# Kernel tuning notes

Measured on AMD Instinct MI355X. Metric: run time of the kernel, lower is better.

Reference implementation:

```python
import jax, jax.numpy as jnp
import numpy as np

H, DH = 16, 64            # num heads, head dim
D = H * DH                # hidden size 1024
ALPHA, BW, A, R = 1.0, 1.0, 0.5, 1.0
D_INT = DH                # num_heads > 1 -> d_intrinsic = head_dim
EPS = 1e-12
CLIP = 1.0 - 1e-6         # keep acos (and its grad) finite


def setup_inputs() -> dict:
    key = jax.random.key(0)
    ks = jax.random.split(key, 5)
    w = lambda k: jax.random.normal(k, (D, D), jnp.float32) * 0.02
    return {
        "x": jax.random.normal(ks[0], (4, 1024, D), jnp.float32),
        "wq": w(ks[1]), "bq": jnp.zeros((D,), jnp.float32),
        "wk": w(ks[2]), "bk": jnp.zeros((D,), jnp.float32),
        "wv": w(ks[3]), "bv": jnp.zeros((D,), jnp.float32),
        "wo": w(ks[4]), "bo": jnp.zeros((D,), jnp.float32),
    }


def reference(x, wq, bq, wk, bk, wv, bv, wo, bo):
    B, S, _ = x.shape

    def heads(t):  # [B,S,D] -> [B,H,S,DH]
        return t.reshape(B, S, H, DH).transpose(0, 2, 1, 3)

    def l2norm(t):
        return t / jnp.maximum(jnp.linalg.norm(t, axis=-1, keepdims=True), EPS)

    q = l2norm(heads(x @ wq + bq))
    k = l2norm(heads(x @ wk + bk))
    v = heads(x @ wv + bv)

    # spherical geodesic distance
    dot = jnp.clip(jnp.einsum('bhqd,bhkd->bhqk', q, k), -CLIP, CLIP)
    g_dist = jnp.arccos(dot) * R

    # power-law kernel (alpha < 2 branch)
    attn_score = (1.0 + g_dist / jnp.sqrt(BW)) ** (-(D_INT + ALPHA))

    # bistochastic (Sinkhorn-like) normalization, a > 0 branch
    n_r = attn_score.sum(-1)   # [B,H,S] row sums
    n_c = attn_score.sum(-2)   # [B,H,S] col sums
    k_tilde = (n_r ** (-A))[..., :, None] * attn_score * (n_c ** (-A))[..., None, :]
    probs = k_tilde / jnp.maximum(k_tilde.sum(-1, keepdims=True), EPS)  # L1 row normalize

    out = jnp.einsum('bhqk,bhkd->bhqd', probs, v)
    out = out.transpose(0, 2, 1, 3).reshape(B, S, D)
    return out @ wo + bo
```

## Files before the change

kernel.cpp:

```cpp
#include <hip/hip_runtime.h>
#include <hip/hip_bf16.h>
#include <cstdint>
#include <cstddef>

#define BATCH  4
#define SEQ    1024
#define NHEAD  16
#define DHEAD  64
#define DMODEL 1024
#define NROWS  4096
#define BH     64
#define CLIPV  0.999999f
#define PEXP   65.0f

#define QOFF   133.5f
#define QK_    490.8988764f
#define QINV   0.0020370716f
#define QC     65535.5f

typedef _Float16 h16;
typedef _Float16 half8 __attribute__((ext_vector_type(8)));
typedef _Float16 half4 __attribute__((ext_vector_type(4)));
typedef __fp16   fp16x2 __attribute__((ext_vector_type(2)));
typedef float    f32x4 __attribute__((ext_vector_type(4)));

typedef const __attribute__((address_space(1))) void gas_void;
typedef __attribute__((address_space(3))) void las_void;
#define GLOAD_LDS16(g, l) \
    __builtin_amdgcn_global_load_lds((gas_void*)(g), (las_void*)(l), 16, 0, 0)

__device__ __forceinline__ float spfns_lg(float d) {
    d = __builtin_amdgcn_fmed3f(d, -CLIPV, CLIPV);
    float a = fabsf(d);
    float s = __builtin_amdgcn_sqrtf(1.0f - a);
    float p = -0.0012624911f;
    p = fmaf(p, a,  0.0066700901f);
    p = fmaf(p, a, -0.0170881256f);
    p = fmaf(p, a,  0.0308918810f);
    p = fmaf(p, a, -0.0501743046f);
    p = fmaf(p, a,  0.0889789874f);
    p = fmaf(p, a, -0.2145988016f);
    p = fmaf(p, a,  1.5707963050f);
    float r = s * p;
    float g = (d >= 0.0f) ? r : (3.14159265358979f - r);
    return __builtin_amdgcn_logf(1.0f + g);
}

__device__ __forceinline__ unsigned pk_h2(float lo, float hi) {
    fp16x2 v = __builtin_amdgcn_cvt_pkrtz(lo, hi);
    return __builtin_bit_cast(unsigned, v);
}

__global__ __launch_bounds__(256) void cvt_x(const float* __restrict__ x,
                                             h16* __restrict__ xh)
{
    size_t i = ((size_t)blockIdx.x * 256 + threadIdx.x) * 8;
    float4 a = *reinterpret_cast<const float4*>(&x[i]);
    float4 b = *reinterpret_cast<const float4*>(&x[i + 4]);
    half8 o;
    o[0]=(h16)a.x; o[1]=(h16)a.y; o[2]=(h16)a.z; o[3]=(h16)a.w;
    o[4]=(h16)b.x; o[5]=(h16)b.y; o[6]=(h16)b.z; o[7]=(h16)b.w;
    *reinterpret_cast<half8*>(&xh[i]) = o;
}

__global__ __launch_bounds__(256) void wtrans(const float* __restrict__ wq,
                                              const float* __restrict__ wk,
                                              const float* __restrict__ wv,
                                              const float* __restrict__ wo,
                                              h16* __restrict__ wt3,
                                              h16* __restrict__ wot)
{
    __shared__ float T[64][65];
    const int k0 = blockIdx.x * 64, d0 = blockIdx.y * 64, z = blockIdx.z;
    const float* src = (z==0)?wq:(z==1)?wk:(z==2)?wv:wo;
    h16* dst = (z==3) ? wot : (wt3 + (size_t)z * 1024 * 1024);
    const int t = threadIdx.x;

    #pragma unroll
    for (int p = 0; p < 4; ++p) {
        int k = (t >> 4) + p * 16;
        int c = (t & 15) * 4;
        float4 v = *reinterpret_cast<const float4*>(&src[(size_t)(k0 + k) * 1024 + d0 + c]);
        T[c + 0][k] = v.x; T[c + 1][k] = v.y; T[c + 2][k] = v.z; T[c + 3][k] = v.w;
    }
    __syncthreads();
    #pragma unroll
    for (int p = 0; p < 2; ++p) {
        int dl = (t >> 3) + p * 32;
        int c  = (t & 7) * 8;
        half8 o;
        #pragma unroll
        for (int e = 0; e < 8; ++e) o[e] = (h16)T[dl][c + e];
        *reinterpret_cast<half8*>(&dst[(size_t)(d0 + dl) * 1024 + k0 + c]) = o;
    }
}

__global__ __launch_bounds__(256) void gemm_f16(const h16* __restrict__ A,
                                                const h16* __restrict__ Bt,
                                                const float* __restrict__ b0,
                                                const float* __restrict__ b1,
                                                const float* __restrict__ b2,
                                                h16* __restrict__ oq,
                                                h16* __restrict__ ok,
                                                h16* __restrict__ ovt,
                                                float* __restrict__ of32,
                                                int mode)
{
    __shared__ __align__(16) h16 As[128][64];
    __shared__ __align__(16) h16 Bs[128][64];
    const int n0 = blockIdx.x * 128, d0 = blockIdx.y * 128;
    const int t = threadIdx.x, l = t & 63, w = t >> 6;
    const int wr = (w >> 1) * 64, wc = (w & 1) * 64;
    const int lr = l >> 3, lc8 = (l & 7) * 8;

    f32x4 acc[4][4];
    #pragma unroll
    for (int i = 0; i < 4; ++i)
        #pragma unroll
        for (int j = 0; j < 4; ++j) acc[i][j] = (f32x4){0.f,0.f,0.f,0.f};

    for (int k0 = 0; k0 < 1024; k0 += 64) {
        __syncthreads();
        #pragma unroll
        for (int q = 0; q < 4; ++q) {
            int r = w * 32 + q * 8;
            GLOAD_LDS16(&A[(size_t)(n0 + r + lr) * 1024 + k0 + lc8], &As[r][0]);
            GLOAD_LDS16(&Bt[(size_t)(d0 + r + lr) * 1024 + k0 + lc8], &Bs[r][0]);
        }
        __syncthreads();
        #pragma unroll
        for (int kk = 0; kk < 2; ++kk) {
            half8 a[4], b[4];
            #pragma unroll
            for (int fi = 0; fi < 4; ++fi)
                a[fi] = *reinterpret_cast<const half8*>(&As[wr + fi*16 + (l & 15)][((l >> 4) * 8) + kk * 32]);
            #pragma unroll
            for (int fj = 0; fj < 4; ++fj)
                b[fj] = *reinterpret_cast<const half8*>(&Bs[wc + fj*16 + (l & 15)][((l >> 4) * 8) + kk * 32]);
            #pragma unroll
            for (int fi = 0; fi < 4; ++fi)
                #pragma unroll
                for (int fj = 0; fj < 4; ++fj)
                    acc[fi][fj] = __builtin_amdgcn_mfma_f32_16x16x32_f16(a[fi], b[fj], acc[fi][fj], 0, 0, 0);
        }
    }

    #pragma unroll
    for (int fi = 0; fi < 4; ++fi) {
        #pragma unroll
        for (int fj = 0; fj < 4; ++fj) {
            int d = d0 + wc + fj * 16 + (l & 15);
            int s0n = n0 + wr + fi * 16 + ((l >> 4) << 2);
            if (mode == 0) {
                int mat = d >> 10, d1 = d & 1023, h = d1 >> 6, dh = d1 & 63;
                const float* bp = (mat == 0) ? b0 : (mat == 1) ? b1 : b2;
                float bias = bp[d1];
                if (mat == 2) {
                    int b = s0n >> 10, s0 = s0n & 1023;
                    half4 o;
                    #pragma unroll
                    for (int rr = 0; rr < 4; ++rr) o[rr] = (h16)(acc[fi][fj][rr] + bias);
                    *reinterpret_cast<half4*>(&ovt[(((size_t)(b * NHEAD + h)) * DHEAD + dh) * SEQ + s0]) = o;
                } else {
                    h16* dst = (mat == 0) ? oq : ok;
                    #pragma unroll
                    for (int rr = 0; rr < 4; ++rr) {
                        int n = s0n + rr, b = n >> 10, s = n & 1023;
                        dst[(((size_t)(b * NHEAD + h)) * SEQ + s) * DHEAD + dh] = (h16)(acc[fi][fj][rr] + bias);
                    }
                }
            } else {
                float bias = b0[d];
                #pragma unroll
                for (int rr = 0; rr < 4; ++rr) {
                    int n = s0n + rr;
                    of32[(size_t)n * DMODEL + d] = acc[fi][fj][rr] + bias;
                }
            }
        }
    }
}

__global__ __launch_bounds__(256) void l2norm_f16(h16* __restrict__ buf)
{
    const int t = threadIdx.x;
    size_t row = (size_t)blockIdx.x * 16 + (t >> 4);
    int c = (t & 15) * 4;
    half4 v = *reinterpret_cast<const half4*>(&buf[row * 64 + c]);
    float f0 = (float)v[0], f1 = (float)v[1], f2 = (float)v[2], f3 = (float)v[3];
    float s = f0*f0 + f1*f1 + f2*f2 + f3*f3;
    #pragma unroll
    for (int off = 1; off < 16; off <<= 1) s += __shfl_xor(s, off);
    float sc = __builtin_amdgcn_rcpf(fmaxf(__builtin_amdgcn_sqrtf(s), 1e-12f));
    half4 o;
    o[0] = (h16)(f0 * sc); o[1] = (h16)(f1 * sc); o[2] = (h16)(f2 * sc); o[3] = (h16)(f3 * sc);
    *reinterpret_cast<half4*>(&buf[row * 64 + c]) = o;
}

template<int CACHED>
__global__ __launch_bounds__(256) void passA(const h16* __restrict__ qh,
                                             const h16* __restrict__ kh,
                                             float* __restrict__ nc,
                                             unsigned* __restrict__ rm_u,
                                             int* __restrict__ gacc,
                                             unsigned short* __restrict__ Sw)
{
    __shared__ __align__(16) h16 Ks[32][72];
    __shared__ float red[4][32];
    const int t = threadIdx.x, l = t & 63, w = t >> 6;
    const int id  = blockIdx.y * 32 + blockIdx.x;
    const int nid = (id & 7) * 256 + (id >> 3);
    const int jt = nid & 31, bh = nid >> 5;
    const int j0 = jt * 32;

    {
        int r = t >> 3, c = (t & 7) * 8;
        *reinterpret_cast<half8*>(&Ks[r][c]) =
            *reinterpret_cast<const half8*>(&kh[(((size_t)bh * SEQ) + j0 + r) * DHEAD + c]);
    }
    __syncthreads();

    half8 kfr[2][2];
    #pragma unroll
    for (int f = 0; f < 2; ++f)
        #pragma unroll
        for (int kk = 0; kk < 2; ++kk)
            kfr[f][kk] = *reinterpret_cast<const half8*>(&Ks[f*16 + (l & 15)][((l >> 4) * 8) + kk * 32]);

    float ncacc[8];
    #pragma unroll
    for (int x = 0; x < 8; ++x) ncacc[x] = 0.f;

    const h16* qb = qh + ((size_t)bh * SEQ + w*16 + (l & 15)) * DHEAD + ((l >> 4) * 8);
    half8 nq0 = *reinterpret_cast<const half8*>(qb);
    half8 nq1 = *reinterpret_cast<const half8*>(qb + 32);

    for (int it = 0; it < 16; ++it) {
        half8 aq0 = nq0, aq1 = nq1;
        if (it < 15) {
            const h16* qn = qb + (size_t)(it + 1) * 64 * DHEAD;
            nq0 = *reinterpret_cast<const half8*>(qn);
            nq1 = *reinterpret_cast<const half8*>(qn + 32);
        }

        float mloc = 1e30f;
        #pragma unroll
        for (int f = 0; f < 2; ++f) {
            f32x4 cfr = (f32x4){0.f,0.f,0.f,0.f};
            cfr = __builtin_amdgcn_mfma_f32_16x16x32_f16(kfr[f][0], aq0, cfr, 0, 0, 0);
            cfr = __builtin_amdgcn_mfma_f32_16x16x32_f16(kfr[f][1], aq1, cfr, 0, 0, 0);
            unsigned uq[4];
            #pragma unroll
            for (int rr = 0; rr < 4; ++rr) {
                float lg = spfns_lg(cfr[rr]);
                float tt = lg * (-PEXP);
                ncacc[f*4 + rr] += __builtin_amdgcn_exp2f(tt);
                mloc = fminf(mloc, lg);
                if (CACHED) uq[rr] = (unsigned)fmaf(tt, QK_, QC);
            }
            if (CACHED) {
                uint2 pkw;
                pkw.x = uq[0] | (uq[1] << 16);
                pkw.y = uq[2] | (uq[3] << 16);
                size_t sidx = (((((size_t)(bh*16 + (jt >> 1))*16 + it)*4 + w)*4
                               + ((jt & 1)*2 + f)) << 8) + (size_t)l*4;
                *reinterpret_cast<uint2*>(&Sw[sidx]) = pkw;
            }
        }
        mloc = fminf(mloc, __shfl_xor(mloc, 16));
        mloc = fminf(mloc, __shfl_xor(mloc, 32));
        if (l < 16)
            atomicMin(&rm_u[(size_t)bh * SEQ + it*64 + w*16 + l], __float_as_uint(mloc));
    }

    #pragma unroll
    for (int x = 0; x < 8; ++x) {
        #pragma unroll
        for (int off = 1; off < 16; off <<= 1)
            ncacc[x] += __shfl_xor(ncacc[x], off);
    }
    if ((l & 15) == 0) {
        #pragma unroll
        for (int x = 0; x < 8; ++x)
            red[w][(x >> 2) * 16 + (l >> 4) * 4 + (x & 3)] = ncacc[x];
    }
    __syncthreads();
    if (t < 32) {
        float v = red[0][t] + red[1][t] + red[2][t] + red[3][t];
        nc[(size_t)bh * SEQ + j0 + t] = v;
        atomicAdd(gacc, (int)rintf(__builtin_amdgcn_logf(v) * 64.0f));
    }
}

__global__ __launch_bounds__(256) void ncprep(const float* __restrict__ nc,
                                              const unsigned* __restrict__ rm_u,
                                              const int* __restrict__ gacc,
                                              float* __restrict__ lcr,
                                              float* __restrict__ lrm)
{
    int i = blockIdx.x * 256 + threadIdx.x;
    float Lm = (float)(*gacc) / (65536.0f * 64.0f);
    lcr[i] = -0.5f * (__builtin_amdgcn_logf(nc[i]) - Lm);
    lrm[i] = -PEXP * __uint_as_float(rm_u[i]);
}

__global__ __launch_bounds__(256) void passB_c(const h16* __restrict__ vt,
                                               const float* __restrict__ lcr,
                                               const float* __restrict__ lrm,
                                               const unsigned short* __restrict__ Sw,
                                               h16* __restrict__ aoh)
{
    __shared__ __align__(16) h16 Vs[64][72];
    __shared__ __align__(16) h16 Ps[4][16][72];
    const int t = threadIdx.x, l = t & 63, w = t >> 6;
    const int id  = blockIdx.y * 16 + blockIdx.x;
    const int nid = (id & 7) * 128 + (id >> 3);
    const int it = nid & 15, bh = nid >> 4;
    const int i0 = it * 64;

    const float nlr = -lrm[(size_t)bh * SEQ + i0 + w*16 + (l & 15)] - QOFF;

    half8 ones8;
    {
        h16 ov = (h16)(((l & 15) == 0) ? 1.0f : 0.0f);
        #pragma unroll
        for (int e = 0; e < 8; ++e) ones8[e] = ov;
    }

    f32x4 pv[4];
    #pragma unroll
    for (int fd = 0; fd < 4; ++fd) pv[fd] = (f32x4){0.f,0.f,0.f,0.f};
    f32x4 pvden = (f32x4){0.f,0.f,0.f,0.f};

    const int sr = t >> 3, sc = (t & 7) * 8;
    const h16* vsrc = vt + ((size_t)bh * DHEAD + sr) * SEQ + sc;
    const float* lc_base = lcr + (size_t)bh * SEQ + (l >> 4) * 4;

    auto s_ptr = [&](int jc2, int fj) -> const uint2* {
        size_t sidx = (((((size_t)(bh*16 + jc2)*16 + it)*4 + w)*4 + fj) << 8) + (size_t)l*4;
        return reinterpret_cast<const uint2*>(&Sw[sidx]);
    };

    half8 vr0 = *reinterpret_cast<const half8*>(vsrc);
    half8 vr1 = *reinterpret_cast<const half8*>(vsrc + (size_t)32 * SEQ);
    uint2 sv[4];
    float4 lc[4];
    #pragma unroll
    for (int fj = 0; fj < 4; ++fj) {
        sv[fj] = *s_ptr(0, fj);
        lc[fj] = *reinterpret_cast<const float4*>(&lc_base[fj*16]);
    }

    for (int jc = 0; jc < 16; ++jc) {
        __syncthreads();
        *reinterpret_cast<half8*>(&Vs[sr][sc])      = vr0;
        *reinterpret_cast<half8*>(&Vs[sr + 32][sc]) = vr1;
        __syncthreads();

        if (jc < 15) {
            const h16* vn = vsrc + (jc + 1) * 64;
            vr0 = *reinterpret_cast<const half8*>(vn);
            vr1 = *reinterpret_cast<const half8*>(vn + (size_t)32 * SEQ);
        }

        #pragma unroll
        for (int fj = 0; fj < 4; ++fj) {
            float u0 = (float)(sv[fj].x & 0xffffu), u1 = (float)(sv[fj].x >> 16);
            float u2 = (float)(sv[fj].y & 0xffffu), u3 = (float)(sv[fj].y >> 16);
            float pp0 = __builtin_amdgcn_exp2f(fmaf(u0, QINV, lc[fj].x + nlr));
            float pp1 = __builtin_amdgcn_exp2f(fmaf(u1, QINV, lc[fj].y + nlr));
            float pp2 = __builtin_amdgcn_exp2f(fmaf(u2, QINV, lc[fj].z + nlr));
            float pp3 = __builtin_amdgcn_exp2f(fmaf(u3, QINV, lc[fj].w + nlr));
            uint2 pk;
            pk.x = pk_h2(pp0, pp1);
            pk.y = pk_h2(pp2, pp3);
            *reinterpret_cast<uint2*>(&Ps[w][l & 15][fj*16 + (l >> 4) * 4]) = pk;
        }
        if (jc < 15) {
            #pragma unroll
            for (int fj = 0; fj < 4; ++fj) {
                sv[fj] = *s_ptr(jc + 1, fj);
                lc[fj] = *reinterpret_cast<const float4*>(&lc_base[(jc + 1)*64 + fj*16]);
            }
        }

        half8 pa0 = *reinterpret_cast<const half8*>(&Ps[w][l & 15][((l >> 4) * 8)]);
        half8 pa1 = *reinterpret_cast<const half8*>(&Ps[w][l & 15][((l >> 4) * 8) + 32]);
        #pragma unroll
        for (int fd = 0; fd < 4; ++fd) {
            half8 vb0 = *reinterpret_cast<const half8*>(&Vs[fd*16 + (l & 15)][((l >> 4) * 8)]);
            half8 vb1 = *reinterpret_cast<const half8*>(&Vs[fd*16 + (l & 15)][((l >> 4) * 8) + 32]);
            pv[fd] = __builtin_amdgcn_mfma_f32_16x16x32_f16(pa0, vb0, pv[fd], 0, 0, 0);
            pv[fd] = __builtin_amdgcn_mfma_f32_16x16x32_f16(pa1, vb1, pv[fd], 0, 0, 0);
        }
        pvden = __builtin_amdgcn_mfma_f32_16x16x32_f16(pa0, ones8, pvden, 0, 0, 0);
        pvden = __builtin_amdgcn_mfma_f32_16x16x32_f16(pa1, ones8, pvden, 0, 0, 0);
    }

    const int b = bh >> 4, h = bh & 15;
    #pragma unroll
    for (int rr = 0; rr < 4; ++rr) {
        float ds = __shfl(pvden[rr], l & 48);
        float inv = __builtin_amdgcn_rcpf(ds);
        int s = i0 + w * 16 + ((l >> 4) << 2) + rr;
        #pragma unroll
        for (int fd = 0; fd < 4; ++fd) {
            aoh[((size_t)(b * SEQ + s)) * DMODEL + h * DHEAD + fd * 16 + (l & 15)] =
                (h16)(pv[fd][rr] * inv);
        }
    }
}

__global__ __launch_bounds__(256) void passB_r(const h16* __restrict__ qh,
                                               const h16* __restrict__ kh,
                                               const h16* __restrict__ vt,
                                               const float* __restrict__ lcr,
                                               const float* __restrict__ lrm,
                                               h16* __restrict__ aoh)
{
    __shared__ __align__(16) h16 Ks[64][72];
    __shared__ __align__(16) h16 Vs[64][72];
    __shared__ __align__(16) h16 Ps[4][16][72];
    __shared__ float lcr_s[64];
    __shared__ float lrm_s[64];

    const int it = blockIdx.x, bh = blockIdx.y;
    const int i0 = it * 64;
    const int t = threadIdx.x, l = t & 63, w = t >> 6;
    h16* Pflat = &Ps[0][0][0];

    #pragma unroll
    for (int p = 0; p < 2; ++p) {
        int r = (t >> 3) + p * 32, c = (t & 7) * 8;
        *reinterpret_cast<half8*>(&Pflat[r * 72 + c]) =
            *reinterpret_cast<const half8*>(&qh[(((size_t)bh * SEQ) + i0 + r) * DHEAD + c]);
    }
    if (t < 64) lrm_s[t] = lrm[(size_t)bh * SEQ + i0 + t];
    __syncthreads();

    half8 aq0 = *reinterpret_cast<const half8*>(&Pflat[(w*16 + (l & 15)) * 72 + ((l >> 4) * 8)]);
    half8 aq1 = *reinterpret_cast<const half8*>(&Pflat[(w*16 + (l & 15)) * 72 + ((l >> 4) * 8) + 32]);
    const float nlr = -lrm_s[w*16 + (l & 15)];

    half8 ones8;
    {
        h16 ov = (h16)(((l & 15) == 0) ? 1.0f : 0.0f);
        #pragma unroll
        for (int e = 0; e < 8; ++e) ones8[e] = ov;
    }

    f32x4 pv[4];
    #pragma unroll
    for (int fd = 0; fd < 4; ++fd) pv[fd] = (f32x4){0.f,0.f,0.f,0.f};
    f32x4 pvden = (f32x4){0.f,0.f,0.f,0.f};

    for (int jc = 0; jc < 16; ++jc) {
        const int j0 = jc * 64;
        __syncthreads();
        #pragma unroll
        for (int p = 0; p < 2; ++p) {
            int r = (t >> 3) + p * 32, c = (t & 7) * 8;
            *reinterpret_cast<half8*>(&Ks[r][c]) =
                *reinterpret_cast<const half8*>(&kh[(((size_t)bh * SEQ) + j0 + r) * DHEAD + c]);
            *reinterpret_cast<half8*>(&Vs[r][c]) =
                *reinterpret_cast<const half8*>(&vt[(((size_t)bh * DHEAD) + r) * SEQ + j0 + c]);
        }
        if (t < 64) lcr_s[t] = lcr[(size_t)bh * SEQ + j0 + t];
        __syncthreads();

        #pragma unroll
        for (int fj = 0; fj < 4; ++fj) {
            half8 kb0 = *reinterpret_cast<const half8*>(&Ks[fj*16 + (l & 15)][((l >> 4) * 8)]);
            half8 kb1 = *reinterpret_cast<const half8*>(&Ks[fj*16 + (l & 15)][((l >> 4) * 8) + 32]);
            f32x4 cfr = (f32x4){0.f,0.f,0.f,0.f};
            cfr = __builtin_amdgcn_mfma_f32_16x16x32_f16(kb0, aq0, cfr, 0, 0, 0);
            cfr = __builtin_amdgcn_mfma_f32_16x16x32_f16(kb1, aq1, cfr, 0, 0, 0);
            float4 lc4 = *reinterpret_cast<const float4*>(&lcr_s[fj*16 + (l >> 4) * 4]);
            float pp0 = __builtin_amdgcn_exp2f(fmaf(spfns_lg(cfr[0]), -PEXP, lc4.x + nlr));
            float pp1 = __builtin_amdgcn_exp2f(fmaf(spfns_lg(cfr[1]), -PEXP, lc4.y + nlr));
            float pp2 = __builtin_amdgcn_exp2f(fmaf(spfns_lg(cfr[2]), -PEXP, lc4.z + nlr));
            float pp3 = __builtin_amdgcn_exp2f(fmaf(spfns_lg(cfr[3]), -PEXP, lc4.w + nlr));
            uint2 pk;
            pk.x = pk_h2(pp0, pp1);
            pk.y = pk_h2(pp2, pp3);
            *reinterpret_cast<uint2*>(&Ps[w][l & 15][fj*16 + (l >> 4) * 4]) = pk;
        }

        half8 pa0 = *reinterpret_cast<const half8*>(&Ps[w][l & 15][((l >> 4) * 8)]);
        half8 pa1 = *reinterpret_cast<const half8*>(&Ps[w][l & 15][((l >> 4) * 8) + 32]);
        #pragma unroll
        for (int fd = 0; fd < 4; ++fd) {
            half8 vb0 = *reinterpret_cast<const half8*>(&Vs[fd*16 + (l & 15)][((l >> 4) * 8)]);
            half8 vb1 = *reinterpret_cast<const half8*>(&Vs[fd*16 + (l & 15)][((l >> 4) * 8) + 32]);
            pv[fd] = __builtin_amdgcn_mfma_f32_16x16x32_f16(pa0, vb0, pv[fd], 0, 0, 0);
            pv[fd] = __builtin_amdgcn_mfma_f32_16x16x32_f16(pa1, vb1, pv[fd], 0, 0, 0);
        }
        pvden = __builtin_amdgcn_mfma_f32_16x16x32_f16(pa0, ones8, pvden, 0, 0, 0);
        pvden = __builtin_amdgcn_mfma_f32_16x16x32_f16(pa1, ones8, pvden, 0, 0, 0);
    }

    const int b = bh >> 4, h = bh & 15;
    #pragma unroll
    for (int rr = 0; rr < 4; ++rr) {
        float ds = __shfl(pvden[rr], l & 48);
        float inv = __builtin_amdgcn_rcpf(ds);
        int s = i0 + w * 16 + ((l >> 4) << 2) + rr;
        #pragma unroll
        for (int fd = 0; fd < 4; ++fd) {
            aoh[((size_t)(b * SEQ + s)) * DMODEL + h * DHEAD + fd * 16 + (l & 15)] =
                (h16)(pv[fd][rr] * inv);
        }
    }
}

extern "C" void kernel_launch(void* const* d_in, const int* in_sizes, int n_in,
                              void* d_out, int out_size, void* d_ws, size_t ws_size,
                              hipStream_t stream)
{
    (void)in_sizes; (void)n_in; (void)out_size;
    const float* x  = (const float*)d_in[0];
    const float* wq = (const float*)d_in[1];
    const float* bq = (const float*)d_in[2];
    const float* wk = (const float*)d_in[3];
    const float* bk = (const float*)d_in[4];
    const float* wv = (const float*)d_in[5];
    const float* bv = (const float*)d_in[6];
    const float* wo = (const float*)d_in[7];
    const float* bo = (const float*)d_in[8];
    float* out = (float*)d_out;

    h16* ws16 = (h16*)d_ws;
    const size_t NX  = (size_t)NROWS * DMODEL;
    const size_t NW3 = (size_t)3 * DMODEL * DMODEL;
    const size_t NW1 = (size_t)DMODEL * DMODEL;
    const size_t NH  = (size_t)BH * SEQ * DHEAD;
    h16* xh  = ws16;
    h16* wt3 = xh  + NX;
    h16* wot = wt3 + NW3;
    h16* qh  = wot + NW1;
    h16* kh  = qh  + NH;
    h16* vt  = kh  + NH;
    h16* aoh = vt  + NH;
    float* nc  = (float*)(aoh + NX);
    float* lcr = nc  + BH * SEQ;
    float* lrm = lcr + BH * SEQ;
    unsigned* rm_u = (unsigned*)(lrm + BH * SEQ);
    int* gacc = (int*)(rm_u + BH * SEQ);

    size_t used = (size_t)((char*)(gacc + 1) - (char*)d_ws);
    used = (used + 255) & ~(size_t)255;
    unsigned short* Sw = (unsigned short*)((char*)d_ws + used);
    const size_t SBYTES = (size_t)BH * SEQ * SEQ * 2;
    const bool cache = (ws_size >= used + SBYTES);

    hipMemsetAsync(rm_u, 0xFF, (size_t)BH * SEQ * sizeof(unsigned), stream);
    hipMemsetAsync(gacc, 0, sizeof(int), stream);

    cvt_x<<<2048, 256, 0, stream>>>(x, xh);
    wtrans<<<dim3(16, 16, 4), 256, 0, stream>>>(wq, wk, wv, wo, wt3, wot);

    gemm_f16<<<dim3(32, 24), 256, 0, stream>>>(xh, wt3, bq, bk, bv,
                                               qh, kh, vt, nullptr, 0);
    l2norm_f16<<<(2 * BH * SEQ) / 16, 256, 0, stream>>>(qh);

    if (cache) {
        passA<1><<<dim3(32, BH), 256, 0, stream>>>(qh, kh, nc, rm_u, gacc, Sw);
        ncprep<<<256, 256, 0, stream>>>(nc, rm_u, gacc, lcr, lrm);
        passB_c<<<dim3(16, BH), 256, 0, stream>>>(vt, lcr, lrm, Sw, aoh);
    } else {
        passA<0><<<dim3(32, BH), 256, 0, stream>>>(qh, kh, nc, rm_u, gacc, Sw);
        ncprep<<<256, 256, 0, stream>>>(nc, rm_u, gacc, lcr, lrm);
        passB_r<<<dim3(16, BH), 256, 0, stream>>>(qh, kh, vt, lcr, lrm, aoh);
    }

    gemm_f16<<<dim3(32, 8), 256, 0, stream>>>(aoh, wot, bo, nullptr, nullptr,
                                              nullptr, nullptr, nullptr, out, 1);
}
```

Before: 193.9 us.

## Fuse L2 norm into QKV GEMM epilogue, shorten acos polynomial, unroll passA

Moves the per-head L2 normalization of q and k into the QKV GEMM epilogue. Each warp tile covers one full 64-wide head, so the sum of squares is reduced with lane shuffles before the fp16 store, and the separate l2norm kernel launch and its read-modify-write pass are removed. Also replaces the 8-term arccos polynomial with a 4-term one to cut ALU work in the score path, at some loss of accuracy. Adds an unroll-2 hint to the passA loop.

```diff
diff --git a/kernel.cpp b/kernel.cpp
--- a/kernel.cpp
+++ b/kernel.cpp
@@ -33,14 +33,10 @@
     d = __builtin_amdgcn_fmed3f(d, -CLIPV, CLIPV);
     float a = fabsf(d);
     float s = __builtin_amdgcn_sqrtf(1.0f - a);
-    float p = -0.0012624911f;
-    p = fmaf(p, a,  0.0066700901f);
-    p = fmaf(p, a, -0.0170881256f);
-    p = fmaf(p, a,  0.0308918810f);
-    p = fmaf(p, a, -0.0501743046f);
-    p = fmaf(p, a,  0.0889789874f);
-    p = fmaf(p, a, -0.2145988016f);
-    p = fmaf(p, a,  1.5707963050f);
+    float p = -0.0187293f;
+    p = fmaf(p, a,  0.0742610f);
+    p = fmaf(p, a, -0.2121144f);
+    p = fmaf(p, a,  1.5707288f);
     float r = s * p;
     float g = (d >= 0.0f) ? r : (3.14159265358979f - r);
     return __builtin_amdgcn_logf(1.0f + g);
@@ -145,31 +141,65 @@
         }
     }
 
-    #pragma unroll
-    for (int fi = 0; fi < 4; ++fi) {
-        #pragma unroll
-        for (int fj = 0; fj < 4; ++fj) {
-            int d = d0 + wc + fj * 16 + (l & 15);
-            int s0n = n0 + wr + fi * 16 + ((l >> 4) << 2);
-            if (mode == 0) {
-                int mat = d >> 10, d1 = d & 1023, h = d1 >> 6, dh = d1 & 63;
-                const float* bp = (mat == 0) ? b0 : (mat == 1) ? b1 : b2;
-                float bias = bp[d1];
+    if (mode == 0) {
+        const int dbase = d0 + wc;
+        const int mat = dbase >> 10, d1b = dbase & 1023, h = d1b >> 6;
+        const float* bp = (mat == 0) ? b0 : (mat == 1) ? b1 : b2;
+        #pragma unroll
+        for (int fi = 0; fi < 4; ++fi) {
+            float vals[4][4];
+            #pragma unroll
+            for (int fj = 0; fj < 4; ++fj) {
+                float bias = bp[d1b + fj * 16 + (l & 15)];
+                #pragma unroll
+                for (int rr = 0; rr < 4; ++rr) vals[fj][rr] = acc[fi][fj][rr] + bias;
+            }
+            if (mat < 2) {
+                float ss[4];
+                #pragma unroll
+                for (int rr = 0; rr < 4; ++rr)
+                    ss[rr] = vals[0][rr]*vals[0][rr] + vals[1][rr]*vals[1][rr]
+                           + vals[2][rr]*vals[2][rr] + vals[3][rr]*vals[3][rr];
+                #pragma unroll
+                for (int off = 1; off < 16; off <<= 1) {
+                    #pragma unroll
+                    for (int rr = 0; rr < 4; ++rr) ss[rr] += __shfl_xor(ss[rr], off);
+                }
+                #pragma unroll
+                for (int rr = 0; rr < 4; ++rr) {
+                    float sc = __builtin_amdgcn_rcpf(
+                        fmaxf(__builtin_amdgcn_sqrtf(ss[rr]), 1e-12f));
+                    #pragma unroll
+                    for (int fj = 0; fj < 4; ++fj) vals[fj][rr] *= sc;
+                }
+            }
+            const int s0n = n0 + wr + fi * 16 + ((l >> 4) << 2);
+            #pragma unroll
+            for (int fj = 0; fj < 4; ++fj) {
+                int dh = fj * 16 + (l & 15);
                 if (mat == 2) {
                     int b = s0n >> 10, s0 = s0n & 1023;
                     half4 o;
                     #pragma unroll
-                    for (int rr = 0; rr < 4; ++rr) o[rr] = (h16)(acc[fi][fj][rr] + bias);
+                    for (int rr = 0; rr < 4; ++rr) o[rr] = (h16)vals[fj][rr];
                     *reinterpret_cast<half4*>(&ovt[(((size_t)(b * NHEAD + h)) * DHEAD + dh) * SEQ + s0]) = o;
                 } else {
                     h16* dst = (mat == 0) ? oq : ok;
                     #pragma unroll
                     for (int rr = 0; rr < 4; ++rr) {
                         int n = s0n + rr, b = n >> 10, s = n & 1023;
-                        dst[(((size_t)(b * NHEAD + h)) * SEQ + s) * DHEAD + dh] = (h16)(acc[fi][fj][rr] + bias);
+                        dst[(((size_t)(b * NHEAD + h)) * SEQ + s) * DHEAD + dh] = (h16)vals[fj][rr];
                     }
                 }
-            } else {
+            }
+        }
+    } else {
+        #pragma unroll
+        for (int fi = 0; fi < 4; ++fi) {
+            #pragma unroll
+            for (int fj = 0; fj < 4; ++fj) {
+                int d = d0 + wc + fj * 16 + (l & 15);
+                int s0n = n0 + wr + fi * 16 + ((l >> 4) << 2);
                 float bias = b0[d];
                 #pragma unroll
                 for (int rr = 0; rr < 4; ++rr) {
@@ -179,22 +209,6 @@
             }
         }
     }
-}
-
-__global__ __launch_bounds__(256) void l2norm_f16(h16* __restrict__ buf)
-{
-    const int t = threadIdx.x;
-    size_t row = (size_t)blockIdx.x * 16 + (t >> 4);
-    int c = (t & 15) * 4;
-    half4 v = *reinterpret_cast<const half4*>(&buf[row * 64 + c]);
-    float f0 = (float)v[0], f1 = (float)v[1], f2 = (float)v[2], f3 = (float)v[3];
-    float s = f0*f0 + f1*f1 + f2*f2 + f3*f3;
-    #pragma unroll
-    for (int off = 1; off < 16; off <<= 1) s += __shfl_xor(s, off);
-    float sc = __builtin_amdgcn_rcpf(fmaxf(__builtin_amdgcn_sqrtf(s), 1e-12f));
-    half4 o;
-    o[0] = (h16)(f0 * sc); o[1] = (h16)(f1 * sc); o[2] = (h16)(f2 * sc); o[3] = (h16)(f3 * sc);
-    *reinterpret_cast<half4*>(&buf[row * 64 + c]) = o;
 }
 
 template<int CACHED>
@@ -235,6 +249,7 @@
     half8 nq0 = *reinterpret_cast<const half8*>(qb);
     half8 nq1 = *reinterpret_cast<const half8*>(qb + 32);
 
+    #pragma unroll 2
     for (int it = 0; it < 16; ++it) {
         half8 aq0 = nq0, aq1 = nq1;
         if (it < 15) {
@@ -561,7 +576,6 @@
 
     gemm_f16<<<dim3(32, 24), 256, 0, stream>>>(xh, wt3, bq, bk, bv,
                                                qh, kh, vt, nullptr, 0);
-    l2norm_f16<<<(2 * BH * SEQ) / 16, 256, 0, stream>>>(qh);
 
     if (cache) {
         passA<1><<<dim3(32, BH), 256, 0, stream>>>(qh, kh, nc, rm_u, gacc, Sw);
```

New measurement: 180.9 us. 6.7% less time.
